# Optimization experiments

Hardware: AMD Instinct MI355X
Metric: run time of the kernel (lower is better)

The kernel has to match this reference:

```python
import jax, jax.numpy as jnp
import numpy as np

DIM = 1024
NUM_HEADS = 16
BATCH = 4
SEQ = 2048
SCALE = (DIM // NUM_HEADS) ** -0.5
MASK_VAL = -10000000.0


def setup_inputs() -> dict:
    key = jax.random.key(0)
    k1, k2, k3, k4 = jax.random.split(key, 4)
    inputs = jax.random.normal(k1, (BATCH, SEQ, DIM), dtype=jnp.float32)
    # xavier-ish scaling for weights
    W_qkv = jax.random.normal(k2, (3 * DIM, DIM), dtype=jnp.float32) * (1.0 / np.sqrt(DIM))
    W_fc = jax.random.normal(k3, (DIM, DIM), dtype=jnp.float32) * (1.0 / np.sqrt(DIM))
    b_fc = jnp.zeros((DIM,), dtype=jnp.float32)
    padding_mask = jax.random.randint(k4, (BATCH, SEQ), 0, 2, dtype=jnp.int32)
    return {"inputs": inputs, "W_qkv": W_qkv, "W_fc": W_fc, "b_fc": b_fc,
            "padding_mask": padding_mask}


def reference(inputs, W_qkv, W_fc, b_fc, padding_mask):
    B, N, C = inputs.shape
    H = NUM_HEADS
    Dh = C // H
    # qkv projection (torch Linear: x @ W.T), [B,N,3C]
    qkv = jnp.einsum('bnc,oc->bno', inputs, W_qkv)
    qkv = qkv.reshape(B, N, 3, H, Dh).transpose(2, 0, 3, 1, 4)  # [3,B,H,N,Dh]
    q, k, v = qkv[0], qkv[1], qkv[2]
    att = jnp.einsum('bhqd,bhkd->bhqk', q, k) * SCALE  # [B,H,N,N]
    mask = padding_mask[:, None, None, :]              # [B,1,1,N]
    att = jnp.where(mask > 0, jnp.float32(MASK_VAL), att)
    att = jax.nn.softmax(att, axis=-1)
    x = jnp.einsum('bhqk,bhkd->bhqd', att, v)          # [B,H,N,Dh]
    x = x.transpose(0, 2, 1, 3).reshape(B, N, C)       # [B,N,C]
    out = jnp.einsum('bnc,oc->bno', x, W_fc) + b_fc
    return out
```

## Files before the change

### kernel.cpp

```cpp
#include <hip/hip_runtime.h>
#include <stdint.h>

constexpr int kDim  = 1024;
constexpr int kH    = 16;
constexpr int kB    = 4;
constexpr int kSeq  = 2048;
constexpr int kDh   = 64;
constexpr int kMTot = kB * kSeq;
constexpr int kNQkv = 3 * kDim;
constexpr float kScale = 0.125f;
constexpr float kLog2e = 1.44269504088896f;
constexpr float kC1    = kScale * kLog2e;
constexpr float kMaxSub = 10.0f;
constexpr float kMk2Un   = -kMaxSub * kLog2e;
constexpr float kMk2Mask = -1.0e9f;
constexpr int kPld = 72;
constexpr int kCld = 136;

typedef __attribute__((ext_vector_type(8))) short short8;
typedef __attribute__((ext_vector_type(4))) float floatx4;

__device__ __forceinline__ unsigned short f2bf(float f) {
  union { float f; unsigned u; } v; v.f = f;
  unsigned r = v.u + 0x7fffu + ((v.u >> 16) & 1u);
  return (unsigned short)(r >> 16);
}
__device__ __forceinline__ unsigned short f2bf_fast(float f) {
  union { float f; unsigned u; } v; v.f = f;
  return (unsigned short)((v.u + 0x8000u) >> 16);
}
__device__ __forceinline__ float vexp2(float x) {
  float r; asm("v_exp_f32 %0, %1" : "=v"(r) : "v"(x)); return r;
}
__device__ __forceinline__ void gl2lds16(const void* g, void* l) {
  __builtin_amdgcn_global_load_lds(
      (const __attribute__((address_space(1))) unsigned int*)g,
      (__attribute__((address_space(3))) unsigned int*)l, 16, 0, 0);
}

__global__ void __launch_bounds__(256) cvt_scan(
    const float4* __restrict__ x, const float4* __restrict__ wq,
    const float4* __restrict__ wf,
    ushort4* __restrict__ xb, ushort4* __restrict__ wqb, ushort4* __restrict__ wfb,
    const int* __restrict__ pm, int* __restrict__ cidx, int* __restrict__ nkd) {
  const int X4  = (kMTot * kDim) / 4;
  const int WQ4 = (kNQkv * kDim) / 4;
  const int NCVT = 12288;
  if (blockIdx.x >= NCVT) {
    const int b = blockIdx.x - NCVT;
    const int t = threadIdx.x;
    const int lane = t & 63, wv = t >> 6;
    __shared__ int wsum[4];
    __shared__ int woff[5];
    int base = t * 8;
    int keep[8]; int cnt = 0;
#pragma unroll
    for (int j = 0; j < 8; j++) {
      keep[j] = (pm[b * kSeq + base + j] <= 0) ? 1 : 0;
      cnt += keep[j];
    }
    int pre = cnt;
#pragma unroll
    for (int off = 1; off < 64; off <<= 1) {
      int v = __shfl_up(pre, off, 64);
      if (lane >= off) pre += v;
    }
    int excl = pre - cnt;
    if (lane == 63) wsum[wv] = pre;
    __syncthreads();
    if (t == 0) {
      int s = 0;
#pragma unroll
      for (int w = 0; w < 4; w++) { woff[w] = s; s += wsum[w]; }
      woff[4] = s;
      nkd[b] = s;
    }
    __syncthreads();
    const int nk = woff[4];
    int kp = woff[wv] + excl;
#pragma unroll
    for (int j = 0; j < 8; j++) {
      int n = base + j;
      int pos = keep[j] ? kp : nk + (n - kp);
      cidx[b * kSeq + pos] = b * kSeq + n;
      kp += keep[j];
    }
    return;
  }
  int i = blockIdx.x * 256 + threadIdx.x;
  float4 v; ushort4* dst;
  if (i < X4)            { v = x[i];             dst = xb  + i; }
  else if (i < X4 + WQ4) { v = wq[i - X4];       dst = wqb + (i - X4); }
  else                   { v = wf[i - X4 - WQ4]; dst = wfb + (i - X4 - WQ4); }
  ushort4 o;
  o.x = f2bf(v.x); o.y = f2bf(v.y); o.z = f2bf(v.z); o.w = f2bf(v.w);
  *dst = o;
}

__device__ __forceinline__ void gemm128_mainloop(
    const unsigned short* const arow[4], const unsigned short* __restrict__ Bw,
    int tN, unsigned short* As, unsigned short* Bs, floatx4 acc[4][4]) {
  const int t = threadIdx.x;
  const int lane = t & 63, wv = t >> 6;
  const int wm = (wv >> 1) << 6, wn = (wv & 1) << 6;
  const int lrow = lane & 15, quad = lane >> 4, l7 = lane & 7;
  const int srow = t >> 3;
  const int pu8 = (t & 7) * 8;
  const int lu8 = ((t & 7) ^ (srow & 7)) * 8;
  const int off0 = (quad ^ l7) * 8;

  floatx4 zero = {0.f, 0.f, 0.f, 0.f};
#pragma unroll
  for (int mi = 0; mi < 4; mi++)
#pragma unroll
    for (int ni = 0; ni < 4; ni++) acc[mi][ni] = zero;

  for (int k0 = 0; k0 < kDim; k0 += 64) {
#pragma unroll
    for (int p = 0; p < 4; ++p) {
      int r = srow + p * 32;
      gl2lds16(arow[p] + k0 + lu8, As + r * 64 + pu8);
      gl2lds16(Bw + (int64_t)(tN + r) * kDim + k0 + lu8, Bs + r * 64 + pu8);
    }
    __syncthreads();
#pragma unroll
    for (int kk = 0; kk < 64; kk += 32) {
      short8 af[4], bf[4];
#pragma unroll
      for (int mi = 0; mi < 4; mi++)
        af[mi] = *(const short8*)(As + (wm + mi * 16 + lrow) * 64 + (off0 ^ kk));
#pragma unroll
      for (int ni = 0; ni < 4; ni++)
        bf[ni] = *(const short8*)(Bs + (wn + ni * 16 + lrow) * 64 + (off0 ^ kk));
#pragma unroll
      for (int mi = 0; mi < 4; mi++)
#pragma unroll
        for (int ni = 0; ni < 4; ni++)
          acc[mi][ni] = __builtin_amdgcn_mfma_f32_16x16x32_bf16(af[mi], bf[ni], acc[mi][ni], 0, 0, 0);
    }
    __syncthreads();
  }
}

__global__ void __launch_bounds__(256) gemm_qkv(
    const unsigned short* __restrict__ xb, const unsigned short* __restrict__ wqb,
    const int* __restrict__ cidx, const int* __restrict__ nkd,
    unsigned short* __restrict__ qb, unsigned short* __restrict__ kb,
    unsigned short* __restrict__ vtb) {
  const int tN = blockIdx.x * 128, tM = blockIdx.y * 128;
  const int which = tN >> 10;
  if (which != 0) {
    int b = tM >> 11, local = tM & 2047;
    if (local >= nkd[b]) return;
  }
  extern __shared__ __attribute__((aligned(16))) unsigned short smem[];
  unsigned short* As = smem;
  unsigned short* Bs = smem + 128 * 64;
  floatx4 acc[4][4];

  const int t = threadIdx.x, srow = t >> 3;
  const unsigned short* arow[4];
#pragma unroll
  for (int p = 0; p < 4; p++) {
    int r = tM + srow + p * 32;
    int rid = (which == 0) ? r : cidx[r];
    arow[p] = xb + (int64_t)rid * kDim;
  }
  gemm128_mainloop(arow, wqb, tN, As, Bs, acc);

  const int lane = t & 63, wv = t >> 6;
  const int wm = (wv >> 1) << 6, wn = (wv & 1) << 6;
  const int lrow = lane & 15, quad = lane >> 4;
  unsigned short* Cs = smem;
  const bool vblk = (which == 2);
#pragma unroll
  for (int ni = 0; ni < 4; ni++) {
    int c = wn + ni * 16 + lrow;
#pragma unroll
    for (int mi = 0; mi < 4; mi++) {
#pragma unroll
      for (int r = 0; r < 4; r++) {
        int row = wm + mi * 16 + quad * 4 + r;
        unsigned short val = f2bf(acc[mi][ni][r]);
        if (!vblk) Cs[row * kCld + c] = val;
        else       Cs[c * kCld + row] = val;
      }
    }
  }
  __syncthreads();
  const int mj8 = lane >> 3;
  const int chunk = lane & 7;
#pragma unroll
  for (int half = 0; half < 2; half++) {
#pragma unroll
    for (int g = 0; g < 4; g++) {
      int mjr = wv * 32 + g * 8 + mj8;
      short8 vec = *(const short8*)(Cs + mjr * kCld + half * 64 + chunk * 8);
      if (!vblk) {
        int i = tM + mjr;
        int bb = i >> 11, n = i & 2047;
        int o = tN + half * 64 + chunk * 8;
        int h = (o >> 6) & 15;
        int64_t base = (int64_t)((bb << 4) + h) << 17;
        unsigned short* dst = (which == 0 ? qb : kb) + base + (int64_t)n * 64 + (o & 63);
        *(short8*)dst = vec;
      } else {
        int o = tN + mjr;
        int h = (o >> 6) & 15, d = o & 63;
        int bb = tM >> 11;
        int n0 = (tM & 2047) + half * 64 + chunk * 8;
        unsigned short* dst = vtb + (((int64_t)((bb << 4) + h)) << 17)
                              + (int64_t)d * 2048 + n0;
        *(short8*)dst = vec;
      }
    }
  }
}

__global__ void __launch_bounds__(256, 4) attn(
    const unsigned short* __restrict__ qb, const unsigned short* __restrict__ kb,
    const unsigned short* __restrict__ vtb, const int* __restrict__ nkd,
    unsigned short* __restrict__ xab) {
  __shared__ __attribute__((aligned(16))) unsigned short Ks[64 * 64];
  __shared__ __attribute__((aligned(16))) unsigned short Vs[64 * 64];
  __shared__ __attribute__((aligned(16))) unsigned short Ps[4][2][16 * kPld];

  const int t = threadIdx.x, lane = t & 63, wv = t >> 6;
  const int lrow = lane & 15, quad = lane >> 4, l7 = lane & 7;
  const int qblk = blockIdx.x & 15, bh = blockIdx.x >> 4;
  const int b = bh >> 4, h = bh & 15;
  const int q0 = qblk * 128;
  const int srow = t >> 3;
  const int pu8 = (t & 7) * 8;
  const int lu8 = ((t & 7) ^ (srow & 7)) * 8;
  const int off0 = (quad ^ l7) * 8;

  const int nk  = nkd[b];
  const int nkt = (nk + 63) >> 6;

  const unsigned short* Qb0 = qb + ((int64_t)bh * kSeq + q0 + wv * 16 + lrow) * kDh;
  short8 qf[2][2];
  qf[0][0] = *(const short8*)(Qb0 + quad * 8);
  qf[0][1] = *(const short8*)(Qb0 + 32 + quad * 8);
  qf[1][0] = *(const short8*)(Qb0 + 64 * kDh + quad * 8);
  qf[1][1] = *(const short8*)(Qb0 + 64 * kDh + 32 + quad * 8);

  float l_run[2][4];
  floatx4 o_acc[2][4];
  floatx4 zero = {0.f, 0.f, 0.f, 0.f};
#pragma unroll
  for (int t2 = 0; t2 < 2; t2++) {
#pragma unroll
    for (int r = 0; r < 4; r++) l_run[t2][r] = 0.f;
#pragma unroll
    for (int di = 0; di < 4; di++) o_acc[t2][di] = zero;
  }

  const unsigned short* Kbase = kb  + (int64_t)bh * kSeq * kDh;
  const unsigned short* Vbase = vtb + (int64_t)bh * kDh * kSeq;

  for (int kt = 0; kt < nkt; ++kt) {
    const int k0 = kt * 64;
    {
      int r0 = srow, r1 = srow + 32;
      gl2lds16(Kbase + (int64_t)(k0 + r0) * kDh + lu8, Ks + r0 * 64 + pu8);
      gl2lds16(Kbase + (int64_t)(k0 + r1) * kDh + lu8, Ks + r1 * 64 + pu8);
      gl2lds16(Vbase + (int64_t)r0 * kSeq + k0 + lu8,  Vs + r0 * 64 + pu8);
      gl2lds16(Vbase + (int64_t)r1 * kSeq + k0 + lu8,  Vs + r1 * 64 + pu8);
    }
    __syncthreads();

    floatx4 s[2][4];
#pragma unroll
    for (int ni = 0; ni < 4; ni++) {
      const unsigned short* Kr = Ks + (ni * 16 + lrow) * 64;
      short8 kf0 = *(const short8*)(Kr + off0);
      short8 kf1 = *(const short8*)(Kr + (off0 ^ 32));
#pragma unroll
      for (int t2 = 0; t2 < 2; t2++) {
        floatx4 tmp = __builtin_amdgcn_mfma_f32_16x16x32_bf16(qf[t2][0], kf0, zero, 0, 0, 0);
        s[t2][ni]   = __builtin_amdgcn_mfma_f32_16x16x32_bf16(qf[t2][1], kf1, tmp, 0, 0, 0);
      }
    }
    float mk2[4];
#pragma unroll
    for (int c = 0; c < 4; c++)
      mk2[c] = (k0 + c * 16 + lrow < nk) ? kMk2Un : kMk2Mask;

#pragma unroll
    for (int t2 = 0; t2 < 2; t2++) {
      unsigned short* Pw = &Ps[wv][t2][0];
#pragma unroll
      for (int r = 0; r < 4; r++) {
        int prow = (quad * 4 + r) * kPld + lrow;
#pragma unroll
        for (int c = 0; c < 4; c++) {
          float p = vexp2(fmaf(s[t2][c][r], kC1, mk2[c]));
          l_run[t2][r] += p;
          Pw[prow + c * 16] = f2bf_fast(p);
        }
      }
    }
    asm volatile("s_waitcnt lgkmcnt(0)" ::: "memory");

#pragma unroll
    for (int ks = 0; ks < 2; ks++) {
      short8 pf0 = *(const short8*)(&Ps[wv][0][0] + lrow * kPld + ks * 32 + quad * 8);
      short8 pf1 = *(const short8*)(&Ps[wv][1][0] + lrow * kPld + ks * 32 + quad * 8);
      const int voff = off0 ^ (ks * 32);
#pragma unroll
      for (int di = 0; di < 4; di++) {
        short8 vf = *(const short8*)(Vs + (di * 16 + lrow) * 64 + voff);
        o_acc[0][di] = __builtin_amdgcn_mfma_f32_16x16x32_bf16(pf0, vf, o_acc[0][di], 0, 0, 0);
        o_acc[1][di] = __builtin_amdgcn_mfma_f32_16x16x32_bf16(pf1, vf, o_acc[1][di], 0, 0, 0);
      }
    }
    __syncthreads();
  }

#pragma unroll
  for (int t2 = 0; t2 < 2; t2++) {
#pragma unroll
    for (int r = 0; r < 4; r++) {
      float l = l_run[t2][r];
      l += __shfl_xor(l, 1, 64);
      l += __shfl_xor(l, 2, 64);
      l += __shfl_xor(l, 4, 64);
      l += __shfl_xor(l, 8, 64);
      float inv = 1.0f / l;
      int n = q0 + t2 * 64 + wv * 16 + quad * 4 + r;
      int64_t rowbase = ((int64_t)b * kSeq + n) * kDim + h * kDh;
#pragma unroll
      for (int di = 0; di < 4; di++)
        xab[rowbase + di * 16 + lrow] = f2bf(o_acc[t2][di][r] * inv);
    }
  }
}

__global__ void __launch_bounds__(256) gemm_fc(
    const unsigned short* __restrict__ xab, const unsigned short* __restrict__ wfb,
    const float* __restrict__ bfc, float* __restrict__ out) {
  __shared__ __attribute__((aligned(16))) unsigned short As[128 * 64];
  __shared__ __attribute__((aligned(16))) unsigned short Bs[64 * 64];
  const int tN = blockIdx.x * 64, tM = blockIdx.y * 128;
  const int t = threadIdx.x;
  const int lane = t & 63, wv = t >> 6;
  const int wm = (wv >> 1) << 6, wn = (wv & 1) << 5;
  const int lrow = lane & 15, quad = lane >> 4, l7 = lane & 7;
  const int srow = t >> 3;
  const int pu8 = (t & 7) * 8;
  const int lu8 = ((t & 7) ^ (srow & 7)) * 8;
  const int off0 = (quad ^ l7) * 8;

  floatx4 acc[4][2];
  floatx4 zero = {0.f, 0.f, 0.f, 0.f};
#pragma unroll
  for (int mi = 0; mi < 4; mi++)
#pragma unroll
    for (int ni = 0; ni < 2; ni++) acc[mi][ni] = zero;

  for (int k0 = 0; k0 < kDim; k0 += 64) {
#pragma unroll
    for (int p = 0; p < 4; ++p) {
      int r = srow + p * 32;
      gl2lds16(xab + (int64_t)(tM + r) * kDim + k0 + lu8, As + r * 64 + pu8);
    }
#pragma unroll
    for (int p = 0; p < 2; ++p) {
      int r = srow + p * 32;
      gl2lds16(wfb + (int64_t)(tN + r) * kDim + k0 + lu8, Bs + r * 64 + pu8);
    }
    __syncthreads();
#pragma unroll
    for (int kk = 0; kk < 64; kk += 32) {
      short8 af[4], bf[2];
#pragma unroll
      for (int mi = 0; mi < 4; mi++)
        af[mi] = *(const short8*)(As + (wm + mi * 16 + lrow) * 64 + (off0 ^ kk));
#pragma unroll
      for (int ni = 0; ni < 2; ni++)
        bf[ni] = *(const short8*)(Bs + (wn + ni * 16 + lrow) * 64 + (off0 ^ kk));
#pragma unroll
      for (int mi = 0; mi < 4; mi++)
#pragma unroll
        for (int ni = 0; ni < 2; ni++)
          acc[mi][ni] = __builtin_amdgcn_mfma_f32_16x16x32_bf16(af[mi], bf[ni], acc[mi][ni], 0, 0, 0);
    }
    __syncthreads();
  }

#pragma unroll
  for (int ni = 0; ni < 2; ni++) {
    int o = tN + wn + ni * 16 + lrow;
    float bias = bfc[o];
#pragma unroll
    for (int mi = 0; mi < 4; mi++) {
#pragma unroll
      for (int r = 0; r < 4; r++) {
        int i = tM + wm + mi * 16 + quad * 4 + r;
        out[(int64_t)i * kDim + o] = acc[mi][ni][r] + bias;
      }
    }
  }
}

extern "C" void kernel_launch(void* const* d_in, const int* in_sizes, int n_in,
                              void* d_out, int out_size, void* d_ws, size_t ws_size,
                              hipStream_t stream) {
  (void)in_sizes; (void)n_in; (void)out_size; (void)ws_size;
  const float* x    = (const float*)d_in[0];
  const float* wqkv = (const float*)d_in[1];
  const float* wfc  = (const float*)d_in[2];
  const float* bfc  = (const float*)d_in[3];
  const int*   pm   = (const int*)d_in[4];
  float* out = (float*)d_out;

  char* ws = (char*)d_ws;
  unsigned short* xb  = (unsigned short*)(ws);
  unsigned short* wqb = (unsigned short*)(ws + 16777216);
  unsigned short* wfb = (unsigned short*)(ws + 23068672);
  unsigned short* qb  = (unsigned short*)(ws + 25165824);
  unsigned short* kb  = (unsigned short*)(ws + 41943040);
  unsigned short* vtb = (unsigned short*)(ws + 58720256);
  int*            cidx= (int*)(ws + 75497472);
  int*            nkd = (int*)(ws + 75530240);
  unsigned short* xab = xb;

  cvt_scan<<<12288 + kB, 256, 0, stream>>>(
      (const float4*)x, (const float4*)wqkv, (const float4*)wfc,
      (ushort4*)xb, (ushort4*)wqb, (ushort4*)wfb, pm, cidx, nkd);
  gemm_qkv<<<dim3(kNQkv / 128, kMTot / 128), 256, 128 * kCld * 2, stream>>>(
      xb, wqb, cidx, nkd, qb, kb, vtb);
  attn<<<kB * kH * (kSeq / 128), 256, 0, stream>>>(qb, kb, vtb, nkd, xab);
  gemm_fc<<<dim3(kDim / 64, kMTot / 128), 256, 0, stream>>>(xab, wfb, bfc, out);
}
```

Before: 256.2 us.

## Rewrite QKV GEMM as 256x256 tile with double-buffered LDS pipeline

Replaces the 128x128 single-buffered QKV GEMM with a 256x256 tile, 512 threads and two LDS buffers (128KB dynamic shared memory). Global-to-LDS loads for the next K tile are interleaved with the MFMA quarters, using manual vmcnt waits, raw barriers and setprio. The aim is to hide load latency and raise arithmetic intensity per block. The cost is heavy register and LDS use, which limits occupancy, plus a more complex two-pass epilogue that writes half the columns per pass.

```diff
diff --git a/kernel.cpp b/kernel.cpp
--- a/kernel.cpp
+++ b/kernel.cpp
@@ -97,124 +97,196 @@
   *dst = o;
 }
 
-__device__ __forceinline__ void gemm128_mainloop(
-    const unsigned short* const arow[4], const unsigned short* __restrict__ Bw,
-    int tN, unsigned short* As, unsigned short* Bs, floatx4 acc[4][4]) {
+__global__ void __launch_bounds__(512, 2) gemm_qkv(
+    const unsigned short* __restrict__ xb, const unsigned short* __restrict__ wqb,
+    const int* __restrict__ cidx, const int* __restrict__ nkd,
+    unsigned short* __restrict__ qb, unsigned short* __restrict__ kb,
+    unsigned short* __restrict__ vtb) {
+  const int tN = blockIdx.x * 256, tM = blockIdx.y * 256;
+  const int which = tN >> 10;
+  const int b = tM >> 11, tMloc = tM & 2047;
+  if (which != 0) {
+    if (tMloc >= nkd[b]) return;
+  }
+  extern __shared__ __attribute__((aligned(16))) unsigned short smem[];
+  unsigned short* As0 = smem;
+  unsigned short* Bs0 = smem + 16384;
+  unsigned short* As1 = smem + 32768;
+  unsigned short* Bs1 = smem + 49152;
+
   const int t = threadIdx.x;
   const int lane = t & 63, wv = t >> 6;
-  const int wm = (wv >> 1) << 6, wn = (wv & 1) << 6;
+  const int wm = (wv >> 2) << 7;
+  const int wn = (wv & 3) << 6;
   const int lrow = lane & 15, quad = lane >> 4, l7 = lane & 7;
   const int srow = t >> 3;
   const int pu8 = (t & 7) * 8;
   const int lu8 = ((t & 7) ^ (srow & 7)) * 8;
   const int off0 = (quad ^ l7) * 8;
 
+  const unsigned short* arow[4];
+#pragma unroll
+  for (int p = 0; p < 4; p++) {
+    int r = tM + srow + p * 64;
+    int rid = (which == 0) ? r : cidx[r];
+    arow[p] = xb + (int64_t)rid * kDim + lu8;
+  }
+  const unsigned short* brow = wqb + (int64_t)(tN + srow) * kDim + lu8;
+
+  floatx4 acc[8][4];
   floatx4 zero = {0.f, 0.f, 0.f, 0.f};
 #pragma unroll
-  for (int mi = 0; mi < 4; mi++)
+  for (int mi = 0; mi < 8; mi++)
 #pragma unroll
     for (int ni = 0; ni < 4; ni++) acc[mi][ni] = zero;
 
-  for (int k0 = 0; k0 < kDim; k0 += 64) {
-#pragma unroll
-    for (int p = 0; p < 4; ++p) {
-      int r = srow + p * 32;
-      gl2lds16(arow[p] + k0 + lu8, As + r * 64 + pu8);
-      gl2lds16(Bw + (int64_t)(tN + r) * kDim + k0 + lu8, Bs + r * 64 + pu8);
-    }
-    __syncthreads();
-#pragma unroll
-    for (int kk = 0; kk < 64; kk += 32) {
-      short8 af[4], bf[4];
-#pragma unroll
-      for (int mi = 0; mi < 4; mi++)
-        af[mi] = *(const short8*)(As + (wm + mi * 16 + lrow) * 64 + (off0 ^ kk));
-#pragma unroll
-      for (int ni = 0; ni < 4; ni++)
-        bf[ni] = *(const short8*)(Bs + (wn + ni * 16 + lrow) * 64 + (off0 ^ kk));
-#pragma unroll
-      for (int mi = 0; mi < 4; mi++)
-#pragma unroll
-        for (int ni = 0; ni < 4; ni++)
-          acc[mi][ni] = __builtin_amdgcn_mfma_f32_16x16x32_bf16(af[mi], bf[ni], acc[mi][ni], 0, 0, 0);
-    }
-    __syncthreads();
-  }
-}
-
-__global__ void __launch_bounds__(256) gemm_qkv(
-    const unsigned short* __restrict__ xb, const unsigned short* __restrict__ wqb,
-    const int* __restrict__ cidx, const int* __restrict__ nkd,
-    unsigned short* __restrict__ qb, unsigned short* __restrict__ kb,
-    unsigned short* __restrict__ vtb) {
-  const int tN = blockIdx.x * 128, tM = blockIdx.y * 128;
-  const int which = tN >> 10;
-  if (which != 0) {
-    int b = tM >> 11, local = tM & 2047;
-    if (local >= nkd[b]) return;
-  }
-  extern __shared__ __attribute__((aligned(16))) unsigned short smem[];
-  unsigned short* As = smem;
-  unsigned short* Bs = smem + 128 * 64;
-  floatx4 acc[4][4];
-
-  const int t = threadIdx.x, srow = t >> 3;
-  const unsigned short* arow[4];
-#pragma unroll
-  for (int p = 0; p < 4; p++) {
-    int r = tM + srow + p * 32;
-    int rid = (which == 0) ? r : cidx[r];
-    arow[p] = xb + (int64_t)rid * kDim;
-  }
-  gemm128_mainloop(arow, wqb, tN, As, Bs, acc);
-
-  const int lane = t & 63, wv = t >> 6;
-  const int wm = (wv >> 1) << 6, wn = (wv & 1) << 6;
-  const int lrow = lane & 15, quad = lane >> 4;
+#define STAGE_B(buf, p, k0) gl2lds16(brow + (int64_t)(p) * 64 * kDim + (k0), \
+                                     (buf) + ((p) * 64 + srow) * 64 + pu8)
+#define STAGE_A(buf, p, k0) gl2lds16(arow[p] + (k0), \
+                                     (buf) + ((p) * 64 + srow) * 64 + pu8)
+#define BARRIER() { asm volatile("" ::: "memory"); \
+                    __builtin_amdgcn_s_barrier(); \
+                    asm volatile("" ::: "memory"); }
+#define LDA(q) { \
+    const unsigned short* Ar0_ = Ac + (wm + (2*(q)) * 16 + lrow) * 64; \
+    const unsigned short* Ar1_ = Ac + (wm + (2*(q)+1) * 16 + lrow) * 64; \
+    af00 = *(const short8*)(Ar0_ + off0); \
+    af01 = *(const short8*)(Ar0_ + (off0 ^ 32)); \
+    af10 = *(const short8*)(Ar1_ + off0); \
+    af11 = *(const short8*)(Ar1_ + (off0 ^ 32)); }
+#define MFMAQ(q) { \
+    __builtin_amdgcn_s_setprio(1); \
+    _Pragma("unroll") \
+    for (int ni = 0; ni < 4; ni++) { \
+      acc[2*(q)][ni]   = __builtin_amdgcn_mfma_f32_16x16x32_bf16(af00, bfr[ni][0], acc[2*(q)][ni],   0, 0, 0); \
+      acc[2*(q)+1][ni] = __builtin_amdgcn_mfma_f32_16x16x32_bf16(af10, bfr[ni][0], acc[2*(q)+1][ni], 0, 0, 0); \
+    } \
+    _Pragma("unroll") \
+    for (int ni = 0; ni < 4; ni++) { \
+      acc[2*(q)][ni]   = __builtin_amdgcn_mfma_f32_16x16x32_bf16(af01, bfr[ni][1], acc[2*(q)][ni],   0, 0, 0); \
+      acc[2*(q)+1][ni] = __builtin_amdgcn_mfma_f32_16x16x32_bf16(af11, bfr[ni][1], acc[2*(q)+1][ni], 0, 0, 0); \
+    } \
+    __builtin_amdgcn_s_setprio(0); }
+
+  STAGE_B(Bs0, 0, 0); STAGE_B(Bs0, 1, 0); STAGE_B(Bs0, 2, 0); STAGE_B(Bs0, 3, 0);
+  STAGE_A(As0, 0, 0); STAGE_A(As0, 2, 0); STAGE_A(As0, 1, 0); STAGE_A(As0, 3, 0);
+  asm volatile("s_waitcnt vmcnt(2)" ::: "memory");
+  BARRIER();
+
+  for (int tt = 0; tt < 16; ++tt) {
+    unsigned short* Ac = (tt & 1) ? As1 : As0;
+    unsigned short* Bc = (tt & 1) ? Bs1 : Bs0;
+    unsigned short* An = (tt & 1) ? As0 : As1;
+    unsigned short* Bn = (tt & 1) ? Bs0 : Bs1;
+    const int kn = (tt + 1) * 64;
+    const bool more = (tt < 15);
+
+    short8 bfr[4][2];
+    short8 af00, af01, af10, af11;
+
+#pragma unroll
+    for (int ni = 0; ni < 4; ni++) {
+      const unsigned short* Br_ = Bc + (wn + ni * 16 + lrow) * 64;
+      bfr[ni][0] = *(const short8*)(Br_ + off0);
+      bfr[ni][1] = *(const short8*)(Br_ + (off0 ^ 32));
+    }
+    LDA(0);
+    if (more) { STAGE_B(Bn, 0, kn); STAGE_B(Bn, 1, kn); }
+    BARRIER();
+    MFMAQ(0);
+    BARRIER();
+    LDA(1);
+    if (more) { STAGE_B(Bn, 2, kn); STAGE_B(Bn, 3, kn); }
+    BARRIER();
+    MFMAQ(1);
+    if (more) { asm volatile("s_waitcnt vmcnt(4)" ::: "memory"); }
+    else      { asm volatile("s_waitcnt vmcnt(0)" ::: "memory"); }
+    BARRIER();
+    LDA(2);
+    if (more) { STAGE_A(An, 0, kn); STAGE_A(An, 2, kn); }
+    BARRIER();
+    MFMAQ(2);
+    BARRIER();
+    LDA(3);
+    if (more) { STAGE_A(An, 1, kn); STAGE_A(An, 3, kn); }
+    BARRIER();
+    MFMAQ(3);
+    asm volatile("s_waitcnt vmcnt(2)" ::: "memory");
+    BARRIER();
+  }
+#undef STAGE_B
+#undef STAGE_A
+#undef LDA
+#undef MFMAQ
+
   unsigned short* Cs = smem;
   const bool vblk = (which == 2);
-#pragma unroll
-  for (int ni = 0; ni < 4; ni++) {
-    int c = wn + ni * 16 + lrow;
-#pragma unroll
-    for (int mi = 0; mi < 4; mi++) {
-#pragma unroll
-      for (int r = 0; r < 4; r++) {
-        int row = wm + mi * 16 + quad * 4 + r;
-        unsigned short val = f2bf(acc[mi][ni][r]);
-        if (!vblk) Cs[row * kCld + c] = val;
-        else       Cs[c * kCld + row] = val;
-      }
-    }
-  }
-  __syncthreads();
-  const int mj8 = lane >> 3;
-  const int chunk = lane & 7;
-#pragma unroll
-  for (int half = 0; half < 2; half++) {
-#pragma unroll
-    for (int g = 0; g < 4; g++) {
-      int mjr = wv * 32 + g * 8 + mj8;
-      short8 vec = *(const short8*)(Cs + mjr * kCld + half * 64 + chunk * 8);
-      if (!vblk) {
-        int i = tM + mjr;
-        int bb = i >> 11, n = i & 2047;
-        int o = tN + half * 64 + chunk * 8;
-        int h = (o >> 6) & 15;
-        int64_t base = (int64_t)((bb << 4) + h) << 17;
-        unsigned short* dst = (which == 0 ? qb : kb) + base + (int64_t)n * 64 + (o & 63);
-        *(short8*)dst = vec;
-      } else {
-        int o = tN + mjr;
-        int h = (o >> 6) & 15, d = o & 63;
-        int bb = tM >> 11;
-        int n0 = (tM & 2047) + half * 64 + chunk * 8;
-        unsigned short* dst = vtb + (((int64_t)((bb << 4) + h)) << 17)
-                              + (int64_t)d * 2048 + n0;
-        *(short8*)dst = vec;
-      }
-    }
-  }
+  const int h4 = (tN >> 6) & 15;
+#pragma unroll
+  for (int h = 0; h < 2; h++) {
+    const bool writer = (((wv & 3) >> 1) == h);
+    const int cwn = (wv & 1) * 64;
+    if (!vblk) {
+      if (writer) {
+#pragma unroll
+        for (int mi = 0; mi < 8; mi++)
+#pragma unroll
+          for (int ni = 0; ni < 4; ni++)
+#pragma unroll
+            for (int r = 0; r < 4; r++) {
+              int row = wm + mi * 16 + quad * 4 + r;
+              int c = cwn + ni * 16 + lrow;
+              Cs[row * kCld + c] = f2bf(acc[mi][ni][r]);
+            }
+      }
+      asm volatile("s_waitcnt lgkmcnt(0)" ::: "memory");
+      BARRIER();
+      unsigned short* qk = (which == 0) ? qb : kb;
+#pragma unroll
+      for (int g = 0; g < 2; g++) {
+        int hh = (h4 + h * 2 + g) & 15;
+        unsigned short* base = qk + ((int64_t)((b << 4) + hh) << 17)
+                               + (int64_t)tMloc * 64;
+#pragma unroll
+        for (int it = 0; it < 4; it++) {
+          int off = it * 4096 + t * 8;
+          int n = off >> 6;
+          int d = off & 63;
+          *(short8*)(base + off) = *(const short8*)(Cs + n * kCld + g * 64 + d);
+        }
+      }
+      BARRIER();
+    } else {
+      if (writer) {
+#pragma unroll
+        for (int mi = 0; mi < 8; mi++)
+#pragma unroll
+          for (int ni = 0; ni < 4; ni++)
+#pragma unroll
+            for (int r = 0; r < 4; r++) {
+              int row = wm + mi * 16 + quad * 4 + r;
+              int c = cwn + ni * 16 + lrow;
+              Cs[c * 264 + row] = f2bf(acc[mi][ni][r]);
+            }
+      }
+      asm volatile("s_waitcnt lgkmcnt(0)" ::: "memory");
+      BARRIER();
+#pragma unroll
+      for (int g = 0; g < 2; g++) {
+        int hh = (h4 + h * 2 + g) & 15;
+        unsigned short* vbase = vtb + ((int64_t)((b << 4) + hh) << 17) + tMloc;
+#pragma unroll
+        for (int it = 0; it < 4; it++) {
+          int off = it * 512 + t;
+          int d = off >> 5, c8 = off & 31;
+          *(short8*)(vbase + (int64_t)d * 2048 + c8 * 8) =
+              *(const short8*)(Cs + (g * 64 + d) * 264 + c8 * 8);
+        }
+      }
+      BARRIER();
+    }
+  }
+#undef BARRIER
 }
 
 __global__ void __launch_bounds__(256, 4) attn(
@@ -426,10 +498,17 @@
   int*            nkd = (int*)(ws + 75530240);
   unsigned short* xab = xb;
 
+  static bool s_attr_set = false;
+  if (!s_attr_set) {
+    (void)hipFuncSetAttribute((const void*)gemm_qkv,
+                              hipFuncAttributeMaxDynamicSharedMemorySize, 131072);
+    s_attr_set = true;
+  }
+
   cvt_scan<<<12288 + kB, 256, 0, stream>>>(
       (const float4*)x, (const float4*)wqkv, (const float4*)wfc,
       (ushort4*)xb, (ushort4*)wqb, (ushort4*)wfb, pm, cidx, nkd);
-  gemm_qkv<<<dim3(kNQkv / 128, kMTot / 128), 256, 128 * kCld * 2, stream>>>(
+  gemm_qkv<<<dim3(kNQkv / 256, kMTot / 256), 512, 131072, stream>>>(
       xb, wqb, cidx, nkd, qb, kb, vtb);
   attn<<<kB * kH * (kSeq / 128), 256, 0, stream>>>(qb, kb, vtb, nkd, xab);
   gemm_fc<<<dim3(kDim / 64, kMTot / 128), 256, 0, stream>>>(xab, wfb, bfc, out);
```

Result: faster. 236.7 us (-7.6%).
